# Kernel tuning notes

Measured on AMD Instinct MI355X. Metric: run time of the kernel, lower is better.

Reference implementation:

```python
import jax, jax.numpy as jnp
import numpy as np

D_OUT, D_IN = 4096, 4096
RANK = 64
NNZ = 1_000_000
ALPHA = 1.0


def setup_inputs() -> dict:
    key = jax.random.key(0)
    k1, k2, k3, k4, k5, k6, k7 = jax.random.split(key, 7)
    x = jax.random.normal(k1, (4, 2048, D_IN), dtype=jnp.float32)
    W_inner = jax.random.normal(k2, (D_OUT, D_IN), dtype=jnp.float32) * 0.02
    A = jax.random.normal(k3, (D_OUT, RANK), dtype=jnp.float32) * 0.02
    Bmat = jax.random.normal(k4, (RANK, D_IN), dtype=jnp.float32) * 0.02
    sp_values = jax.random.normal(k5, (NNZ,), dtype=jnp.float32) * 0.02
    rows = jax.random.randint(k6, (NNZ,), 0, D_OUT)
    cols = jax.random.randint(k7, (NNZ,), 0, D_IN)
    sp_indices = jnp.stack([rows, cols]).astype(jnp.int64)
    return {"x": x, "W_inner": W_inner, "A": A, "Bmat": Bmat,
            "sp_values": sp_values, "sp_indices": sp_indices}


def reference(x, W_inner, A, Bmat, sp_values, sp_indices):
    # inner module: dense linear z = x @ W_inner^T  -> [b, s, d_out]
    z = jnp.einsum('bsd,od->bso', x, W_inner)
    # low-rank correction: A @ (B @ x)
    r = jnp.einsum('bsd,rd->bsr', x, Bmat)          # [b, s, rank]
    corr = jnp.einsum('bsr,or->bso', r, A)          # [b, s, d_out]
    # sparse COO correction: coalesce (sum duplicates) then sparse.mm(sp, x^T)^T
    # scatter-add duplicates into a dense [d_out, d_in] matrix (same math as coalesce)
    S = jnp.zeros((D_OUT, D_IN), dtype=x.dtype).at[sp_indices[0], sp_indices[1]].add(sp_values)
    corr = corr + jnp.einsum('bsd,od->bso', x, S)
    return z + ALPHA * corr
```

## Files before the change

kernel.cpp:

```cpp
#include <hip/hip_runtime.h>

#define D_OUT 4096
#define D_IN  4096
#define RANK  64
#define NNZ   1000000
#define MTOT  8192
#define KDIM  4096
#define NDIM  4096

typedef __bf16 bf16_t;
typedef __bf16 bf16x8 __attribute__((ext_vector_type(8)));
typedef __bf16 bf16x4 __attribute__((ext_vector_type(4)));
typedef float  f32x4  __attribute__((ext_vector_type(4)));

__global__ __launch_bounds__(256) void scatter_sp_kernel(
    const float* __restrict__ vals, const int* __restrict__ idx,
    float* __restrict__ S) {
  int i = blockIdx.x * 256 + threadIdx.x;
  if (i < NNZ) {
    int r = idx[i];
    int c = idx[NNZ + i];
    atomicAdd(&S[(size_t)r * D_IN + c], vals[i]);
  }
}

__global__ __launch_bounds__(256) void build_weff_fused_kernel(
    const float* __restrict__ W, const float* __restrict__ A,
    const float* __restrict__ B, const float* __restrict__ S,
    bf16_t* __restrict__ outb) {
  __shared__ float sA[64 * 64];
  const int o0 = blockIdx.y * 64;
  const int d0 = blockIdx.x * 128;
  const int t  = threadIdx.x;
  const int td = t & 31;
  const int to = t >> 5;
  const int d  = d0 + td * 4;

  #pragma unroll
  for (int i = 0; i < 16; ++i)
    sA[t + i * 256] = A[(size_t)o0 * 64 + t + i * 256];
  __syncthreads();

  f32x4 acc[8] = {};
  for (int r = 0; r < 64; ++r) {
    f32x4 bv = *(const f32x4*)&B[(size_t)r * D_IN + d];
    #pragma unroll
    for (int j = 0; j < 8; ++j) {
      float a = sA[(to * 8 + j) * 64 + r];
      acc[j] += a * bv;
    }
  }

  #pragma unroll
  for (int j = 0; j < 8; ++j) {
    int o = o0 + to * 8 + j;
    size_t idx = (size_t)o * D_IN + d;
    f32x4 wv = *(const f32x4*)&W[idx];
    f32x4 sv = *(const f32x4*)&S[idx];
    f32x4 v  = wv + sv + acc[j];
    bf16x4 ob;
    ob[0] = (bf16_t)v[0]; ob[1] = (bf16_t)v[1];
    ob[2] = (bf16_t)v[2]; ob[3] = (bf16_t)v[3];
    *(bf16x4*)&outb[idx] = ob;
  }
}

__global__ __launch_bounds__(256) void cvt_bf16_kernel(
    const float* __restrict__ in, bf16_t* __restrict__ out, int n8) {
  int i = blockIdx.x * 256 + threadIdx.x;
  if (i >= n8) return;
  const f32x4* p = (const f32x4*)in + (size_t)i * 2;
  f32x4 a = p[0], b = p[1];
  bf16x8 o;
  o[0] = (bf16_t)a[0]; o[1] = (bf16_t)a[1]; o[2] = (bf16_t)a[2]; o[3] = (bf16_t)a[3];
  o[4] = (bf16_t)b[0]; o[5] = (bf16_t)b[1]; o[6] = (bf16_t)b[2]; o[7] = (bf16_t)b[3];
  *((bf16x8*)out + i) = o;
}

__global__ __launch_bounds__(256) void gemm_bt_kernel(
    const bf16_t* __restrict__ Xb, const bf16_t* __restrict__ Wb,
    float* __restrict__ out) {
  __shared__ bf16_t lA[128 * 64];
  __shared__ bf16_t lB[128 * 64];

  const int t    = threadIdx.x;
  const int w    = t >> 6;
  const int lane = t & 63;
  const int m0 = blockIdx.y * 128;
  const int n0 = blockIdx.x * 128;
  const int wm = (w >> 1) * 64;
  const int wn = (w & 1) * 64;
  const int lr = lane & 15;
  const int lq = lane >> 4;
  const int h  = lr & 7;

  f32x4 acc[4][4] = {};

  for (int k0 = 0; k0 < KDIM; k0 += 64) {
    #pragma unroll
    for (int j = 0; j < 4; ++j) {
      int f   = j * 256 + t;
      int row = f >> 3;
      int kc  = (((f & 7) ^ (row & 7)) << 3);
      const bf16_t* ga = Xb + (size_t)(m0 + row) * KDIM + k0 + kc;
      const bf16_t* gb = Wb + (size_t)(n0 + row) * KDIM + k0 + kc;
      __builtin_amdgcn_global_load_lds(
          (const __attribute__((address_space(1))) void*)(const void*)ga,
          (__attribute__((address_space(3))) void*)(void*)&lA[f * 8], 16, 0, 0);
      __builtin_amdgcn_global_load_lds(
          (const __attribute__((address_space(1))) void*)(const void*)gb,
          (__attribute__((address_space(3))) void*)(void*)&lB[f * 8], 16, 0, 0);
    }
    __syncthreads();

    #pragma unroll
    for (int kk = 0; kk < 64; kk += 32) {
      bf16x8 af[4], bfr[4];
      #pragma unroll
      for (int i = 0; i < 4; ++i) {
        int cj = (((kk >> 3) + lq) ^ h) << 3;
        af[i] = *(const bf16x8*)&lA[(wm + i * 16 + lr) * 64 + cj];
      }
      #pragma unroll
      for (int j = 0; j < 4; ++j) {
        int cj = (((kk >> 3) + lq) ^ h) << 3;
        bfr[j] = *(const bf16x8*)&lB[(wn + j * 16 + lr) * 64 + cj];
      }
      #pragma unroll
      for (int i = 0; i < 4; ++i)
        #pragma unroll
        for (int j = 0; j < 4; ++j)
          acc[i][j] = __builtin_amdgcn_mfma_f32_16x16x32_bf16(
              af[i], bfr[j], acc[i][j], 0, 0, 0);
    }
    __syncthreads();
  }

  #pragma unroll
  for (int i = 0; i < 4; ++i)
    #pragma unroll
    for (int j = 0; j < 4; ++j)
      #pragma unroll
      for (int rr = 0; rr < 4; ++rr) {
        int mm = m0 + wm + i * 16 + lq * 4 + rr;
        int nn = n0 + wn + j * 16 + lr;
        out[(size_t)mm * NDIM + nn] = acc[i][j][rr];
      }
}

extern "C" void kernel_launch(void* const* d_in, const int* in_sizes, int n_in,
                              void* d_out, int out_size, void* d_ws, size_t ws_size,
                              hipStream_t stream) {
  const float* x  = (const float*)d_in[0];
  const float* W  = (const float*)d_in[1];
  const float* A  = (const float*)d_in[2];
  const float* B  = (const float*)d_in[3];
  const float* sv = (const float*)d_in[4];
  const int*   si = (const int*)d_in[5];
  float* out = (float*)d_out;

  float*  S     = (float*)d_ws;
  bf16_t* weffb = (bf16_t*)(S + (size_t)D_OUT * D_IN);
  bf16_t* xb    = weffb + (size_t)D_OUT * D_IN;

  hipMemsetAsync(S, 0, (size_t)D_OUT * D_IN * sizeof(float), stream);
  scatter_sp_kernel<<<(NNZ + 255) / 256, 256, 0, stream>>>(sv, si, S);
  build_weff_fused_kernel<<<dim3(D_IN / 128, D_OUT / 64), 256, 0, stream>>>(W, A, B, S, weffb);
  cvt_bf16_kernel<<<(MTOT * KDIM / 8) / 256, 256, 0, stream>>>(x, xb, MTOT * KDIM / 8);
  gemm_bt_kernel<<<dim3(NDIM / 128, MTOT / 128), 256, 0, stream>>>(xb, weffb, out);
}
```

Before: 680.0 us.

## Rewrite GEMM as 256x256 double-buffered pipelined kernel with 8 waves

Replaces the 128x128 single-buffered bf16 GEMM with a 256x256 tile kernel using 512 threads and double-buffered LDS. Global-to-LDS loads for the next K tile are issued in quarters between MFMA blocks, with explicit vmcnt and lgkmcnt waits and barriers. It also adds s_setprio around MFMA blocks and a workgroup-id remap for L2 locality. The aim is to overlap memory with matrix math and raise arithmetic intensity. The costs are higher register and LDS pressure (128 KB LDS per block) and fragile hand-written wait counts.

Result: no change. 678.9 us (-0.2%).

```diff
diff --git a/kernel.cpp b/kernel.cpp
--- a/kernel.cpp
+++ b/kernel.cpp
@@ -7,6 +7,11 @@
 #define MTOT  8192
 #define KDIM  4096
 #define NDIM  4096
+
+#define BM 256
+#define BN 256
+#define BK 64
+#define NT (KDIM / BK)
 
 typedef __bf16 bf16_t;
 typedef __bf16 bf16x8 __attribute__((ext_vector_type(8)));
@@ -77,67 +82,123 @@
   *((bf16x8*)out + i) = o;
 }
 
-__global__ __launch_bounds__(256) void gemm_bt_kernel(
+
+#define VMCNT4() asm volatile("s_waitcnt vmcnt(4)" ::: "memory")
+#define VMCNT0() asm volatile("s_waitcnt vmcnt(0)" ::: "memory")
+#define LGKM0()  asm volatile("s_waitcnt lgkmcnt(0)" ::: "memory")
+#define BARR()   do { asm volatile("" ::: "memory"); \
+                      __builtin_amdgcn_s_barrier(); \
+                      asm volatile("" ::: "memory"); } while (0)
+
+__global__ __launch_bounds__(512, 2) void gemm256_kernel(
     const bf16_t* __restrict__ Xb, const bf16_t* __restrict__ Wb,
     float* __restrict__ out) {
-  __shared__ bf16_t lA[128 * 64];
-  __shared__ bf16_t lB[128 * 64];
+  __shared__ bf16_t lds[2][2][4][256 * 16];
 
   const int t    = threadIdx.x;
   const int w    = t >> 6;
   const int lane = t & 63;
-  const int m0 = blockIdx.y * 128;
-  const int n0 = blockIdx.x * 128;
-  const int wm = (w >> 1) * 64;
-  const int wn = (w & 1) * 64;
-  const int lr = lane & 15;
-  const int lq = lane >> 4;
-  const int h  = lr & 7;
-
-  f32x4 acc[4][4] = {};
-
-  for (int k0 = 0; k0 < KDIM; k0 += 64) {
-    #pragma unroll
-    for (int j = 0; j < 4; ++j) {
-      int f   = j * 256 + t;
-      int row = f >> 3;
-      int kc  = (((f & 7) ^ (row & 7)) << 3);
-      const bf16_t* ga = Xb + (size_t)(m0 + row) * KDIM + k0 + kc;
-      const bf16_t* gb = Wb + (size_t)(n0 + row) * KDIM + k0 + kc;
-      __builtin_amdgcn_global_load_lds(
-          (const __attribute__((address_space(1))) void*)(const void*)ga,
-          (__attribute__((address_space(3))) void*)(void*)&lA[f * 8], 16, 0, 0);
-      __builtin_amdgcn_global_load_lds(
-          (const __attribute__((address_space(1))) void*)(const void*)gb,
-          (__attribute__((address_space(3))) void*)(void*)&lB[f * 8], 16, 0, 0);
-    }
-    __syncthreads();
-
-    #pragma unroll
-    for (int kk = 0; kk < 64; kk += 32) {
-      bf16x8 af[4], bfr[4];
-      #pragma unroll
-      for (int i = 0; i < 4; ++i) {
-        int cj = (((kk >> 3) + lq) ^ h) << 3;
-        af[i] = *(const bf16x8*)&lA[(wm + i * 16 + lr) * 64 + cj];
-      }
-      #pragma unroll
-      for (int j = 0; j < 4; ++j) {
-        int cj = (((kk >> 3) + lq) ^ h) << 3;
-        bfr[j] = *(const bf16x8*)&lB[(wn + j * 16 + lr) * 64 + cj];
-      }
-      #pragma unroll
-      for (int i = 0; i < 4; ++i)
-        #pragma unroll
-        for (int j = 0; j < 4; ++j)
-          acc[i][j] = __builtin_amdgcn_mfma_f32_16x16x32_bf16(
-              af[i], bfr[j], acc[i][j], 0, 0, 0);
-    }
-    __syncthreads();
-  }
+  const int lr   = lane & 15;
+  const int lq   = lane >> 4;
+  const int qsel = lq >> 1;
+  const int kh8  = (lq & 1) * 8;
+
+  const int bid  = blockIdx.x;
+  const int wgid = (bid & 7) * 64 + (bid >> 3);
+  const int m0 = (wgid >> 4) * BM;
+  const int n0 = (wgid & 15) * BN;
+
+  const int wm = (w >> 2) * 128;
+  const int wn = (w & 3) * 64;
+
+  const int sr  = t >> 1;
+  const int skh = t & 1;
+  const size_t aBase = (size_t)(m0 + sr) * KDIM + skh * 8;
+  const size_t bBase = (size_t)(n0 + sr) * KDIM + skh * 8;
+
+#define STAGE_A(NXT, TKN, Q)                                                   \
+  __builtin_amdgcn_global_load_lds(                                            \
+      (const __attribute__((address_space(1))) void*)(const void*)             \
+          (Xb + aBase + (size_t)(TKN) * BK + (Q) * 16),                        \
+      (__attribute__((address_space(3))) void*)(void*)&lds[NXT][0][Q][t * 8],  \
+      16, 0, 0)
+#define STAGE_B(NXT, TKN, Q)                                                   \
+  __builtin_amdgcn_global_load_lds(                                            \
+      (const __attribute__((address_space(1))) void*)(const void*)             \
+          (Wb + bBase + (size_t)(TKN) * BK + (Q) * 16),                        \
+      (__attribute__((address_space(3))) void*)(void*)&lds[NXT][1][Q][t * 8],  \
+      16, 0, 0)
+
+#define RD_A(IB, CUR, KS) do {                                                 \
+    _Pragma("unroll")                                                          \
+    for (int i_ = 0; i_ < 4; ++i_)                                             \
+      av[i_] = *(const bf16x8*)&lds[CUR][0][(KS) * 2 + qsel]                   \
+                   [(wm + ((IB) + i_) * 16 + lr) * 16 + kh8];                  \
+  } while (0)
+#define RD_B(CUR, KS) do {                                                     \
+    _Pragma("unroll")                                                          \
+    for (int j_ = 0; j_ < 4; ++j_)                                             \
+      bv[j_] = *(const bf16x8*)&lds[CUR][1][(KS) * 2 + qsel]                   \
+                   [(wn + j_ * 16 + lr) * 16 + kh8];                           \
+  } while (0)
+
+#define MFMA_BLOCK(IB) do {                                                    \
+    __builtin_amdgcn_s_setprio(1);                                             \
+    _Pragma("unroll")                                                          \
+    for (int i_ = 0; i_ < 4; ++i_)                                             \
+      _Pragma("unroll")                                                        \
+      for (int j_ = 0; j_ < 4; ++j_)                                           \
+        acc[(IB) + i_][j_] = __builtin_amdgcn_mfma_f32_16x16x32_bf16(          \
+            av[i_], bv[j_], acc[(IB) + i_][j_], 0, 0, 0);                      \
+    __builtin_amdgcn_s_setprio(0);                                             \
+  } while (0)
+
+#define GEMM_TILE(CUR, NXT, TKN, STG) do {                                     \
+                                                                       \
+    RD_A(0, CUR, 0); RD_B(CUR, 0);                                             \
+    if (STG) { STAGE_A(NXT, TKN, 0); STAGE_B(NXT, TKN, 0); }                   \
+    BARR(); LGKM0(); __builtin_amdgcn_sched_barrier(0);                        \
+    MFMA_BLOCK(0);                                                             \
+    BARR();                                                                    \
+                                                                       \
+    RD_A(4, CUR, 0);                                                           \
+    if (STG) { STAGE_A(NXT, TKN, 1); STAGE_B(NXT, TKN, 1); VMCNT4(); }         \
+    else     { VMCNT0(); }                                                     \
+    BARR(); LGKM0(); __builtin_amdgcn_sched_barrier(0);                        \
+    MFMA_BLOCK(4);                                                             \
+    BARR();                                                                    \
+                                                                       \
+    RD_A(0, CUR, 1); RD_B(CUR, 1);                                             \
+    if (STG) { STAGE_A(NXT, TKN, 2); STAGE_B(NXT, TKN, 2); }                   \
+    BARR(); LGKM0(); __builtin_amdgcn_sched_barrier(0);                        \
+    MFMA_BLOCK(0);                                                             \
+    BARR();                                                                    \
+                                                                       \
+    RD_A(4, CUR, 1);                                                           \
+    if (STG) { STAGE_A(NXT, TKN, 3); STAGE_B(NXT, TKN, 3); VMCNT4(); }         \
+    BARR(); LGKM0(); __builtin_amdgcn_sched_barrier(0);                        \
+    MFMA_BLOCK(4);                                                             \
+    BARR();                                                                    \
+  } while (0)
+
+  f32x4 acc[8][4] = {};
+  bf16x8 av[4], bv[4];
+
+  STAGE_A(0, 0, 0); STAGE_B(0, 0, 0);
+  STAGE_A(0, 0, 1); STAGE_B(0, 0, 1);
+  STAGE_A(0, 0, 2); STAGE_B(0, 0, 2);
+  STAGE_A(0, 0, 3); STAGE_B(0, 0, 3);
+  VMCNT4();
+  BARR();
+
+  for (int tk = 0; tk < NT - 1; ++tk) {
+    const int cur = tk & 1;
+    GEMM_TILE(cur, cur ^ 1, tk + 1, 1);
+  }
+  GEMM_TILE(1, 0, 0, 0);
 
   #pragma unroll
-  for (int i = 0; i < 4; ++i)
+  for (int i = 0; i < 8; ++i)
     #pragma unroll
     for (int j = 0; j < 4; ++j)
       #pragma unroll
@@ -146,6 +207,13 @@
         int nn = n0 + wn + j * 16 + lr;
         out[(size_t)mm * NDIM + nn] = acc[i][j][rr];
       }
+
+#undef STAGE_A
+#undef STAGE_B
+#undef RD_A
+#undef RD_B
+#undef MFMA_BLOCK
+#undef GEMM_TILE
 }
 
 extern "C" void kernel_launch(void* const* d_in, const int* in_sizes, int n_in,
@@ -167,5 +235,5 @@
   scatter_sp_kernel<<<(NNZ + 255) / 256, 256, 0, stream>>>(sv, si, S);
   build_weff_fused_kernel<<<dim3(D_IN / 128, D_OUT / 64), 256, 0, stream>>>(W, A, B, S, weffb);
   cvt_bf16_kernel<<<(MTOT * KDIM / 8) / 256, 256, 0, stream>>>(x, xb, MTOT * KDIM / 8);
-  gemm_bt_kernel<<<dim3(NDIM / 128, MTOT / 128), 256, 0, stream>>>(xb, weffb, out);
-}
+  gemm256_kernel<<<dim3((MTOT / BM) * (NDIM / BN)), 512, 0, stream>>>(xb, weffb, out);
+}
```
